# Kernel optimization log

Measured on AMD Instinct MI355X. Metric: run time of the kernel, lower is better.

The kernel has to match this reference:

```python
import jax, jax.numpy as jnp
import numpy as np

OBS_LEN = 8
B = 262144
H = 16   # lstm hidden / MADE hidden / cond dim
D = 2    # trajectory input dim / flow dim
N_FLOWS = 4
CLAMP = 5.0


def _masks():
    # MADE masks for num_inputs=2, num_hidden=16 (ikostrikov get_mask)
    in_deg = jnp.arange(D) % D                      # [0, 1]
    hid_deg = jnp.zeros((H,), jnp.float32)          # arange(16) % (2-1) == 0
    out_deg = (jnp.arange(2 * D) % D - 1).astype(jnp.float32)  # [-1,0,-1,0]
    input_mask = (hid_deg[:, None] >= in_deg[None, :].astype(jnp.float32)).astype(jnp.float32)  # [16,2]
    hidden_mask = jnp.ones((H, H), jnp.float32)     # all degrees 0 -> full
    output_mask = (out_deg[:, None] >= hid_deg[None, :]).astype(jnp.float32)  # [4,16]
    return input_mask, hidden_mask, output_mask


def _made_ma(x, cond, p, masks):
    # x: [B,2], cond: [B,16] -> m, a: [B,2]
    im, hm, om = masks
    jW, jb, cW, hW, hb, oW, ob = p
    h = x @ (jW * im).T + jb + cond @ cW.T      # joiner (masked) + cond linear (no bias)
    h = jax.nn.relu(h)
    h = jax.nn.relu(h @ (hW * hm).T + hb)       # trunk hidden masked linear
    out = h @ (oW * om).T + ob                  # trunk output masked linear -> [B,4]
    m, a = out[:, :D], out[:, D:]
    a = CLAMP * jnp.tanh(a / CLAMP)             # soft log-scale clamp (clamp_flow)
    return m, a


def _made_inverse(u, cond, p, masks):
    x = jnp.zeros_like(u)
    for i in range(D):
        m, a = _made_ma(x, cond, p, masks)
        x = x.at[:, i].set(u[:, i] * jnp.exp(a[:, i]) + m[:, i])
    return x


def _maf_sample(noise, cond, made_params, masks):
    # modules = [MADE0,Rev,MADE1,Rev,MADE2,Rev,MADE3,Rev]; sample runs inverse in reversed order
    x = noise
    for k in reversed(range(N_FLOWS)):
        x = x[:, ::-1]                           # Reverse(2) inverse == flip
        p = tuple(t[k] for t in made_params)
        x = _made_inverse(x, cond, p, masks)
    return x


def _encode(traj, enc_W, enc_b, W_ih, W_hh, b_ih, b_hh, h0, c0):
    # obs_len LSTM loop; dropout is identity in eval/test mode
    def step(carry, x_t):
        h, c = carry
        e = jax.nn.relu(x_t @ enc_W.T + enc_b)                 # [B,16]
        g = e @ W_ih.T + b_ih + h @ W_hh.T + b_hh              # [B,64]
        i, f, gg, o = jnp.split(g, 4, axis=-1)                 # torch LSTMCell gate order
        c = jax.nn.sigmoid(f) * c + jax.nn.sigmoid(i) * jnp.tanh(gg)
        h = jax.nn.sigmoid(o) * jnp.tanh(c)
        return (h, c), None
    (h, c), _ = jax.lax.scan(step, (h0, c0), traj)
    return h


def setup_inputs() -> dict:
    key = jax.random.key(0)
    ks = jax.random.split(key, 16)
    s = 0.1
    return {
        "traj_rel": jax.random.normal(ks[0], (OBS_LEN + 1, B, D), jnp.float32),
        "obs_traj_pos": jax.random.normal(ks[1], (OBS_LEN, B, D), jnp.float32),
        "h0": jax.random.normal(ks[2], (B, H), jnp.float32),
        "c0": jax.random.normal(ks[3], (B, H), jnp.float32),
        "noise": jax.random.normal(ks[4], (B, D), jnp.float32),
        "enc_W": jax.random.normal(ks[5], (H, D), jnp.float32) * 0.2,
        "enc_b": jnp.zeros((H,), jnp.float32),
        "lstm_W_ih": jax.random.normal(ks[6], (4 * H, H), jnp.float32) * s,
        "lstm_W_hh": jax.random.normal(ks[7], (4 * H, H), jnp.float32) * 0.001,
        "lstm_b_ih": jnp.zeros((4 * H,), jnp.float32).at[H:2 * H].set(1.0),
        "lstm_b_hh": jnp.zeros((4 * H,), jnp.float32),
        "made_joiner_W": jax.random.normal(ks[8], (N_FLOWS, H, D), jnp.float32) * s,
        "made_joiner_b": jnp.zeros((N_FLOWS, H), jnp.float32),
        "made_cond_W": jax.random.normal(ks[9], (N_FLOWS, H, H), jnp.float32) * s,
        "made_hid_W": jax.random.normal(ks[10], (N_FLOWS, H, H), jnp.float32) * s,
        "made_hid_b": jnp.zeros((N_FLOWS, H), jnp.float32),
        "made_out_W": jax.random.normal(ks[11], (N_FLOWS, 2 * D, H), jnp.float32) * s,
        "made_out_b": jnp.zeros((N_FLOWS, 2 * D), jnp.float32),
    }


def reference(traj_rel, obs_traj_pos, h0, c0, noise,
              enc_W, enc_b, lstm_W_ih, lstm_W_hh, lstm_b_ih, lstm_b_hh,
              made_joiner_W, made_joiner_b, made_cond_W,
              made_hid_W, made_hid_b, made_out_W, made_out_b):
    masks = _masks()
    h = _encode(traj_rel[:OBS_LEN], enc_W, enc_b,
                lstm_W_ih, lstm_W_hh, lstm_b_ih, lstm_b_hh, h0, c0)  # [B,16]
    made_params = (made_joiner_W, made_joiner_b, made_cond_W,
                   made_hid_W, made_hid_b, made_out_W, made_out_b)
    goal = _maf_sample(noise, h, made_params, masks)                  # [B,2]
    return goal + obs_traj_pos[-1]                                    # mode='test' output_pred
```

## Files before the change

### kernel.cpp

```cpp
#include <hip/hip_runtime.h>

#define B_N 262144
#define OBS_N 8

typedef __attribute__((ext_vector_type(4))) _Float16 f16x4;
typedef __attribute__((ext_vector_type(2))) __fp16 fp16x2;
typedef __attribute__((ext_vector_type(4))) float f32x4;

#define LOG2E 1.44269504088896340736f

__device__ __forceinline__ float rcpf_(float x){ return __builtin_amdgcn_rcpf(x); }
__device__ __forceinline__ float exp2f_(float x){ return __builtin_amdgcn_exp2f(x); }
__device__ __forceinline__ float expf_(float x){ return exp2f_(LOG2E * x); }
__device__ __forceinline__ float tanh_(float x){ return fmaf(-2.0f, rcpf_(exp2f_((2.0f*LOG2E) * x) + 1.0f), 1.0f); }

__device__ __forceinline__ f16x4 pack4(float a, float b, float c, float d){
    fp16x2 lo = __builtin_amdgcn_cvt_pkrtz(a, b);
    fp16x2 hi = __builtin_amdgcn_cvt_pkrtz(c, d);
    f16x4 r;
    r[0] = (_Float16)lo[0]; r[1] = (_Float16)lo[1];
    r[2] = (_Float16)hi[0]; r[3] = (_Float16)hi[1];
    return r;
}

#define MFMA16(a, b, c) __builtin_amdgcn_mfma_f32_16x16x16f16((a), (b), (c), 0, 0, 0)


__global__ __launch_bounds__(256) void goal_kernel(
    const float* __restrict__ traj,
    const float* __restrict__ obsp,
    const float* __restrict__ h0,
    const float* __restrict__ c0,
    const float* __restrict__ noise,
    const float* __restrict__ encW,
    const float* __restrict__ encb,
    const float* __restrict__ Wih,
    const float* __restrict__ Whh,
    const float* __restrict__ bih,
    const float* __restrict__ bhh,
    const float* __restrict__ jW,
    const float* __restrict__ jb,
    const float* __restrict__ cW,
    const float* __restrict__ hW,
    const float* __restrict__ hb,
    const float* __restrict__ oW,
    const float* __restrict__ ob,
    float* __restrict__ out)
{
    const int lane = threadIdx.x & 63;
    const int wv   = threadIdx.x >> 6;
    const int q    = lane >> 4;
    const int s    = lane & 15;
    const int j4   = q * 4;
    const int base = blockIdx.x * 128 + wv * 32;
    const int colA = base + s;
    const int colB = base + 16 + s;

    float ew0[4], ew1[4], eb[4];
    #pragma unroll
    for (int r = 0; r < 4; ++r) {
        ew0[r] = encW[(j4 + r) * 2 + 0];
        ew1[r] = encW[(j4 + r) * 2 + 1];
        eb[r]  = encb[j4 + r];
    }

    const float gsc[4] = { -LOG2E, -LOG2E, -2.0f*LOG2E, -LOG2E };

    f16x4 wihA[4], whhA[4];
    f32x4 bias[4];
    #pragma unroll
    for (int m = 0; m < 4; ++m) {
        float4 wa = *(const float4*)(Wih + (16 * m + s) * 16 + j4);
        float4 wb = *(const float4*)(Whh + (16 * m + s) * 16 + j4);
        wihA[m] = pack4(wa.x*gsc[m], wa.y*gsc[m], wa.z*gsc[m], wa.w*gsc[m]);
        whhA[m] = pack4(wb.x*gsc[m], wb.y*gsc[m], wb.z*gsc[m], wb.w*gsc[m]);
        float4 b1 = *(const float4*)(bih + 16 * m + j4);
        float4 b2 = *(const float4*)(bhh + 16 * m + j4);
        f32x4 bv;
        bv[0] = (b1.x + b2.x)*gsc[m]; bv[1] = (b1.y + b2.y)*gsc[m];
        bv[2] = (b1.z + b2.z)*gsc[m]; bv[3] = (b1.w + b2.w)*gsc[m];
        bias[m] = bv;
    }

    float ob0c[4], ob1c[4], ob2c[4], ob3c[4], ea0c[4];
    #pragma unroll
    for (int kf = 0; kf < 4; ++kf) {
        ob0c[kf] = ob[kf*4 + 0];
        ob1c[kf] = ob[kf*4 + 1];
        ob2c[kf] = ob[kf*4 + 2];
        ob3c[kf] = ob[kf*4 + 3] * 0.2f;
        ea0c[kf] = expf_(5.0f * tanh_(ob2c[kf] * 0.2f));
    }

    f32x4 cA = *(const f32x4*)(c0 + colA * 16 + j4);
    f32x4 cB = *(const f32x4*)(c0 + colB * 16 + j4);
    float4 hA0 = *(const float4*)(h0 + colA * 16 + j4);
    float4 hB0 = *(const float4*)(h0 + colB * 16 + j4);
    f16x4 hA = pack4(hA0.x, hA0.y, hA0.z, hA0.w);
    f16x4 hB = pack4(hB0.x, hB0.y, hB0.z, hB0.w);

    float2 nzA = *(const float2*)(noise + colA * 2);
    float2 nzB = *(const float2*)(noise + colB * 2);

    float2 xA = *(const float2*)(traj + colA * 2);
    float2 xB = *(const float2*)(traj + colB * 2);

    const float NEG2L2E = -2.0f * LOG2E;

    for (int t = 0; t < OBS_N; ++t) {
        float2 nxA, nxB;
        if (t < OBS_N - 1) {
            nxA = *(const float2*)(traj + (t + 1) * (B_N * 2) + colA * 2);
            nxB = *(const float2*)(traj + (t + 1) * (B_N * 2) + colB * 2);
        }
        float eAv[4], eBv[4];
        #pragma unroll
        for (int r = 0; r < 4; ++r) {
            eAv[r] = fmaxf(fmaf(ew0[r], xA.x, fmaf(ew1[r], xA.y, eb[r])), 0.0f);
            eBv[r] = fmaxf(fmaf(ew0[r], xB.x, fmaf(ew1[r], xB.y, eb[r])), 0.0f);
        }
        f16x4 eA = pack4(eAv[0], eAv[1], eAv[2], eAv[3]);
        f16x4 eB = pack4(eBv[0], eBv[1], eBv[2], eBv[3]);

        f32x4 gA[4], gB[4];
        #pragma unroll
        for (int m = 0; m < 4; ++m) {
            gA[m] = MFMA16(wihA[m], eA, bias[m]);
            gA[m] = MFMA16(whhA[m], hA, gA[m]);
            gB[m] = MFMA16(wihA[m], eB, bias[m]);
            gB[m] = MFMA16(whhA[m], hB, gB[m]);
        }

        float hnA[4], hnB[4];
        #pragma unroll
        for (int r = 0; r < 4; ++r) {
            {
                float Ei = exp2f_(gA[0][r]);
                float Ef = exp2f_(gA[1][r]);
                float Eg = exp2f_(gA[2][r]);
                float Eo = exp2f_(gA[3][r]);
                float pi = 1.0f + Ei, pf = 1.0f + Ef, pg = 1.0f + Eg;
                float m_ = pi * pg;
                float R1 = rcpf_(m_ * pf);
                float cn = fmaf(cA[r], m_, (1.0f - Eg) * pf) * R1;
                cA[r] = cn;
                float Ec = exp2f_(NEG2L2E * cn);
                float R2 = rcpf_((1.0f + Ec) * (1.0f + Eo));
                hnA[r] = (1.0f - Ec) * R2;
            }
            {
                float Ei = exp2f_(gB[0][r]);
                float Ef = exp2f_(gB[1][r]);
                float Eg = exp2f_(gB[2][r]);
                float Eo = exp2f_(gB[3][r]);
                float pi = 1.0f + Ei, pf = 1.0f + Ef, pg = 1.0f + Eg;
                float m_ = pi * pg;
                float R1 = rcpf_(m_ * pf);
                float cn = fmaf(cB[r], m_, (1.0f - Eg) * pf) * R1;
                cB[r] = cn;
                float Ec = exp2f_(NEG2L2E * cn);
                float R2 = rcpf_((1.0f + Ec) * (1.0f + Eo));
                hnB[r] = (1.0f - Ec) * R2;
            }
        }
        hA = pack4(hnA[0], hnA[1], hnA[2], hnA[3]);
        hB = pack4(hnB[0], hnB[1], hnB[2], hnB[3]);

        if (t < OBS_N - 1) { xA = nxA; xB = nxB; }
    }

    float2 ppA = *(const float2*)(obsp + (OBS_N - 1) * (B_N * 2) + colA * 2);
    float2 ppB = *(const float2*)(obsp + (OBS_N - 1) * (B_N * 2) + colB * 2);

    float x0A = nzA.x, x1A = nzA.y;
    float x0B = nzB.x, x1B = nzB.y;

    #pragma unroll
    for (int kf = 3; kf >= 0; --kf) {
        float tA = x0A; x0A = x1A; x1A = tA;
        float tB = x0B; x0B = x1B; x1B = tB;

        float4 cw = *(const float4*)(cW + kf * 256 + s * 16 + j4);
        f16x4 cwA = pack4(cw.x, cw.y, cw.z, cw.w);
        float4 hw = *(const float4*)(hW + kf * 256 + s * 16 + j4);
        f16x4 hwA = pack4(hw.x, hw.y, hw.z, hw.w);
        {
        }
        float osc = ((s & 3) == 3) ? 0.2f : 1.0f;
        float4 ow = *(const float4*)(oW + kf * 64 + (s & 3) * 16 + j4);
        f16x4 owA = pack4(ow.x * osc, ow.y * osc, ow.z * osc, ow.w * osc);

        float jw0[4], jb_[4], hb_[4];
        #pragma unroll
        for (int r = 0; r < 4; ++r) {
            jw0[r] = jW[kf * 32 + (j4 + r) * 2];
            jb_[r] = jb[kf * 16 + j4 + r];
            hb_[r] = hb[kf * 16 + j4 + r];
        }

        x0A = fmaf(x0A, ea0c[kf], ob0c[kf]);
        x0B = fmaf(x0B, ea0c[kf], ob0c[kf]);

        f32x4 a1A, a1B;
        #pragma unroll
        for (int r = 0; r < 4; ++r) {
            a1A[r] = fmaf(jw0[r], x0A, jb_[r]);
            a1B[r] = fmaf(jw0[r], x0B, jb_[r]);
        }
        a1A = MFMA16(cwA, hA, a1A);
        a1B = MFMA16(cwA, hB, a1B);
        f16x4 h1A = pack4(fmaxf(a1A[0],0.f), fmaxf(a1A[1],0.f), fmaxf(a1A[2],0.f), fmaxf(a1A[3],0.f));
        f16x4 h1B = pack4(fmaxf(a1B[0],0.f), fmaxf(a1B[1],0.f), fmaxf(a1B[2],0.f), fmaxf(a1B[3],0.f));

        f32x4 a2A, a2B;
        #pragma unroll
        for (int r = 0; r < 4; ++r) { a2A[r] = hb_[r]; a2B[r] = hb_[r]; }
        a2A = MFMA16(hwA, h1A, a2A);
        a2B = MFMA16(hwA, h1B, a2B);
        f16x4 h2A = pack4(fmaxf(a2A[0],0.f), fmaxf(a2A[1],0.f), fmaxf(a2A[2],0.f), fmaxf(a2A[3],0.f));
        f16x4 h2B = pack4(fmaxf(a2B[0],0.f), fmaxf(a2B[1],0.f), fmaxf(a2B[2],0.f), fmaxf(a2B[3],0.f));

        f32x4 a3A, a3B;
        a3A[0]=ob0c[kf]; a3A[1]=ob1c[kf]; a3A[2]=ob2c[kf]; a3A[3]=ob3c[kf];
        a3B[0]=ob0c[kf]; a3B[1]=ob1c[kf]; a3B[2]=ob2c[kf]; a3B[3]=ob3c[kf];
        a3A = MFMA16(owA, h2A, a3A);
        a3B = MFMA16(owA, h2B, a3B);

        float a1vA = 5.0f * tanh_(a3A[3]);
        float a1vB = 5.0f * tanh_(a3B[3]);
        x1A = fmaf(x1A, expf_(a1vA), a3A[1]);
        x1B = fmaf(x1B, expf_(a1vB), a3B[1]);
    }

    if (q == 0) {
        float2 oA; oA.x = x0A + ppA.x; oA.y = x1A + ppA.y;
        float2 oB; oB.x = x0B + ppB.x; oB.y = x1B + ppB.y;
        *(float2*)(out + colA * 2) = oA;
        *(float2*)(out + colB * 2) = oB;
    }
}

extern "C" void kernel_launch(void* const* d_in, const int* in_sizes, int n_in,
                              void* d_out, int out_size, void* d_ws, size_t ws_size,
                              hipStream_t stream) {
    goal_kernel<<<B_N / 128, 256, 0, stream>>>(
        (const float*)d_in[0],  (const float*)d_in[1],  (const float*)d_in[2],
        (const float*)d_in[3],  (const float*)d_in[4],  (const float*)d_in[5],
        (const float*)d_in[6],  (const float*)d_in[7],  (const float*)d_in[8],
        (const float*)d_in[9],  (const float*)d_in[10], (const float*)d_in[11],
        (const float*)d_in[12], (const float*)d_in[13], (const float*)d_in[14],
        (const float*)d_in[15], (const float*)d_in[16], (const float*)d_in[17],
        (float*)d_out);
}
```

Baseline: 50.22 us.

## Cut register pressure: fp16 encoder math, rolled loops, occupancy launch bound

Adds a launch bound of four blocks per CU and marks the LSTM and flow loops as not unrolled. Encoder weights and gate biases are stored as packed fp16, and the encoder affine plus ReLU runs in packed half math. Per-flow output-bias constants are recomputed inside the flow loop, and the final position load moves into the q==0 branch. The aim is fewer VGPRs and higher occupancy, at the cost of lower encoder precision and lost cross-iteration scheduling freedom from unrolling.

New measurement: 44.32 us, median of 3. 11.8% less time.

```diff
diff --git a/kernel.cpp b/kernel.cpp
--- a/kernel.cpp
+++ b/kernel.cpp
@@ -11,7 +11,6 @@
 
 __device__ __forceinline__ float rcpf_(float x){ return __builtin_amdgcn_rcpf(x); }
 __device__ __forceinline__ float exp2f_(float x){ return __builtin_amdgcn_exp2f(x); }
-__device__ __forceinline__ float expf_(float x){ return exp2f_(LOG2E * x); }
 __device__ __forceinline__ float tanh_(float x){ return fmaf(-2.0f, rcpf_(exp2f_((2.0f*LOG2E) * x) + 1.0f), 1.0f); }
 
 __device__ __forceinline__ f16x4 pack4(float a, float b, float c, float d){
@@ -25,8 +24,7 @@
 
 #define MFMA16(a, b, c) __builtin_amdgcn_mfma_f32_16x16x16f16((a), (b), (c), 0, 0, 0)
 
-
-__global__ __launch_bounds__(256) void goal_kernel(
+__global__ __launch_bounds__(256, 4) void goal_kernel(
     const float* __restrict__ traj,
     const float* __restrict__ obsp,
     const float* __restrict__ h0,
@@ -56,18 +54,17 @@
     const int colA = base + s;
     const int colB = base + 16 + s;
 
-    float ew0[4], ew1[4], eb[4];
+    f16x4 ew0h, ew1h, ebh;
     #pragma unroll
     for (int r = 0; r < 4; ++r) {
-        ew0[r] = encW[(j4 + r) * 2 + 0];
-        ew1[r] = encW[(j4 + r) * 2 + 1];
-        eb[r]  = encb[j4 + r];
+        ew0h[r] = (_Float16)encW[(j4 + r) * 2 + 0];
+        ew1h[r] = (_Float16)encW[(j4 + r) * 2 + 1];
+        ebh[r]  = (_Float16)encb[j4 + r];
     }
 
     const float gsc[4] = { -LOG2E, -LOG2E, -2.0f*LOG2E, -LOG2E };
 
-    f16x4 wihA[4], whhA[4];
-    f32x4 bias[4];
+    f16x4 wihA[4], whhA[4], biasH[4];
     #pragma unroll
     for (int m = 0; m < 4; ++m) {
         float4 wa = *(const float4*)(Wih + (16 * m + s) * 16 + j4);
@@ -76,20 +73,8 @@
         whhA[m] = pack4(wb.x*gsc[m], wb.y*gsc[m], wb.z*gsc[m], wb.w*gsc[m]);
         float4 b1 = *(const float4*)(bih + 16 * m + j4);
         float4 b2 = *(const float4*)(bhh + 16 * m + j4);
-        f32x4 bv;
-        bv[0] = (b1.x + b2.x)*gsc[m]; bv[1] = (b1.y + b2.y)*gsc[m];
-        bv[2] = (b1.z + b2.z)*gsc[m]; bv[3] = (b1.w + b2.w)*gsc[m];
-        bias[m] = bv;
-    }
-
-    float ob0c[4], ob1c[4], ob2c[4], ob3c[4], ea0c[4];
-    #pragma unroll
-    for (int kf = 0; kf < 4; ++kf) {
-        ob0c[kf] = ob[kf*4 + 0];
-        ob1c[kf] = ob[kf*4 + 1];
-        ob2c[kf] = ob[kf*4 + 2];
-        ob3c[kf] = ob[kf*4 + 3] * 0.2f;
-        ea0c[kf] = expf_(5.0f * tanh_(ob2c[kf] * 0.2f));
+        biasH[m] = pack4((b1.x+b2.x)*gsc[m], (b1.y+b2.y)*gsc[m],
+                         (b1.z+b2.z)*gsc[m], (b1.w+b2.w)*gsc[m]);
     }
 
     f32x4 cA = *(const f32x4*)(c0 + colA * 16 + j4);
@@ -102,32 +87,40 @@
     float2 nzA = *(const float2*)(noise + colA * 2);
     float2 nzB = *(const float2*)(noise + colB * 2);
 
+    const float NEG2L2E = -2.0f * LOG2E;
+
     float2 xA = *(const float2*)(traj + colA * 2);
     float2 xB = *(const float2*)(traj + colB * 2);
 
-    const float NEG2L2E = -2.0f * LOG2E;
-
+    #pragma unroll 1
     for (int t = 0; t < OBS_N; ++t) {
         float2 nxA, nxB;
         if (t < OBS_N - 1) {
             nxA = *(const float2*)(traj + (t + 1) * (B_N * 2) + colA * 2);
             nxB = *(const float2*)(traj + (t + 1) * (B_N * 2) + colB * 2);
         }
-        float eAv[4], eBv[4];
+
+        _Float16 ax = (_Float16)xA.x, ay = (_Float16)xA.y;
+        _Float16 bx = (_Float16)xB.x, by = (_Float16)xB.y;
+        f16x4 xxA = { ax, ax, ax, ax }, yyA = { ay, ay, ay, ay };
+        f16x4 xxB = { bx, bx, bx, bx }, yyB = { by, by, by, by };
+        f16x4 eA = ew0h * xxA + ew1h * yyA + ebh;
+        f16x4 eB = ew0h * xxB + ew1h * yyB + ebh;
         #pragma unroll
         for (int r = 0; r < 4; ++r) {
-            eAv[r] = fmaxf(fmaf(ew0[r], xA.x, fmaf(ew1[r], xA.y, eb[r])), 0.0f);
-            eBv[r] = fmaxf(fmaf(ew0[r], xB.x, fmaf(ew1[r], xB.y, eb[r])), 0.0f);
-        }
-        f16x4 eA = pack4(eAv[0], eAv[1], eAv[2], eAv[3]);
-        f16x4 eB = pack4(eBv[0], eBv[1], eBv[2], eBv[3]);
+            eA[r] = eA[r] > (_Float16)0 ? eA[r] : (_Float16)0;
+            eB[r] = eB[r] > (_Float16)0 ? eB[r] : (_Float16)0;
+        }
 
         f32x4 gA[4], gB[4];
         #pragma unroll
         for (int m = 0; m < 4; ++m) {
-            gA[m] = MFMA16(wihA[m], eA, bias[m]);
+            f32x4 bv;
+            bv[0] = (float)biasH[m][0]; bv[1] = (float)biasH[m][1];
+            bv[2] = (float)biasH[m][2]; bv[3] = (float)biasH[m][3];
+            gA[m] = MFMA16(wihA[m], eA, bv);
             gA[m] = MFMA16(whhA[m], hA, gA[m]);
-            gB[m] = MFMA16(wihA[m], eB, bias[m]);
+            gB[m] = MFMA16(wihA[m], eB, bv);
             gB[m] = MFMA16(whhA[m], hB, gB[m]);
         }
 
@@ -139,28 +132,28 @@
                 float Ef = exp2f_(gA[1][r]);
                 float Eg = exp2f_(gA[2][r]);
                 float Eo = exp2f_(gA[3][r]);
-                float pi = 1.0f + Ei, pf = 1.0f + Ef, pg = 1.0f + Eg;
+                float pi = 1.0f + Ei, pg = 1.0f + Eg, pf = 1.0f + Ef;
                 float m_ = pi * pg;
                 float R1 = rcpf_(m_ * pf);
-                float cn = fmaf(cA[r], m_, (1.0f - Eg) * pf) * R1;
+                float cn = fmaf(cA[r], m_, fmaf(-Eg, pf, pf)) * R1;
                 cA[r] = cn;
                 float Ec = exp2f_(NEG2L2E * cn);
                 float R2 = rcpf_((1.0f + Ec) * (1.0f + Eo));
-                hnA[r] = (1.0f - Ec) * R2;
+                hnA[r] = fmaf(-Ec, R2, R2);
             }
             {
                 float Ei = exp2f_(gB[0][r]);
                 float Ef = exp2f_(gB[1][r]);
                 float Eg = exp2f_(gB[2][r]);
                 float Eo = exp2f_(gB[3][r]);
-                float pi = 1.0f + Ei, pf = 1.0f + Ef, pg = 1.0f + Eg;
+                float pi = 1.0f + Ei, pg = 1.0f + Eg, pf = 1.0f + Ef;
                 float m_ = pi * pg;
                 float R1 = rcpf_(m_ * pf);
-                float cn = fmaf(cB[r], m_, (1.0f - Eg) * pf) * R1;
+                float cn = fmaf(cB[r], m_, fmaf(-Eg, pf, pf)) * R1;
                 cB[r] = cn;
                 float Ec = exp2f_(NEG2L2E * cn);
                 float R2 = rcpf_((1.0f + Ec) * (1.0f + Eo));
-                hnB[r] = (1.0f - Ec) * R2;
+                hnB[r] = fmaf(-Ec, R2, R2);
             }
         }
         hA = pack4(hnA[0], hnA[1], hnA[2], hnA[3]);
@@ -169,43 +162,35 @@
         if (t < OBS_N - 1) { xA = nxA; xB = nxB; }
     }
 
-    float2 ppA = *(const float2*)(obsp + (OBS_N - 1) * (B_N * 2) + colA * 2);
-    float2 ppB = *(const float2*)(obsp + (OBS_N - 1) * (B_N * 2) + colB * 2);
-
     float x0A = nzA.x, x1A = nzA.y;
     float x0B = nzB.x, x1B = nzB.y;
 
-    #pragma unroll
+    #pragma unroll 1
     for (int kf = 3; kf >= 0; --kf) {
         float tA = x0A; x0A = x1A; x1A = tA;
         float tB = x0B; x0B = x1B; x1B = tB;
+
+        float ob0 = ob[kf*4 + 0], ob1 = ob[kf*4 + 1];
+        float ob2 = ob[kf*4 + 2], ob3 = ob[kf*4 + 3] * 0.2f;
+        float ea0 = exp2f_(7.2134752044f * tanh_(ob2 * 0.2f));
+        x0A = fmaf(x0A, ea0, ob0);
+        x0B = fmaf(x0B, ea0, ob0);
 
         float4 cw = *(const float4*)(cW + kf * 256 + s * 16 + j4);
         f16x4 cwA = pack4(cw.x, cw.y, cw.z, cw.w);
         float4 hw = *(const float4*)(hW + kf * 256 + s * 16 + j4);
         f16x4 hwA = pack4(hw.x, hw.y, hw.z, hw.w);
-        {
-        }
         float osc = ((s & 3) == 3) ? 0.2f : 1.0f;
         float4 ow = *(const float4*)(oW + kf * 64 + (s & 3) * 16 + j4);
         f16x4 owA = pack4(ow.x * osc, ow.y * osc, ow.z * osc, ow.w * osc);
 
-        float jw0[4], jb_[4], hb_[4];
+        f32x4 a1A, a1B;
         #pragma unroll
         for (int r = 0; r < 4; ++r) {
-            jw0[r] = jW[kf * 32 + (j4 + r) * 2];
-            jb_[r] = jb[kf * 16 + j4 + r];
-            hb_[r] = hb[kf * 16 + j4 + r];
-        }
-
-        x0A = fmaf(x0A, ea0c[kf], ob0c[kf]);
-        x0B = fmaf(x0B, ea0c[kf], ob0c[kf]);
-
-        f32x4 a1A, a1B;
-        #pragma unroll
-        for (int r = 0; r < 4; ++r) {
-            a1A[r] = fmaf(jw0[r], x0A, jb_[r]);
-            a1B[r] = fmaf(jw0[r], x0B, jb_[r]);
+            float jwv = jW[kf * 32 + (j4 + r) * 2];
+            float jbv = jb[kf * 16 + j4 + r];
+            a1A[r] = fmaf(jwv, x0A, jbv);
+            a1B[r] = fmaf(jwv, x0B, jbv);
         }
         a1A = MFMA16(cwA, hA, a1A);
         a1B = MFMA16(cwA, hB, a1B);
@@ -214,25 +199,25 @@
 
         f32x4 a2A, a2B;
         #pragma unroll
-        for (int r = 0; r < 4; ++r) { a2A[r] = hb_[r]; a2B[r] = hb_[r]; }
+        for (int r = 0; r < 4; ++r) { float hbv = hb[kf * 16 + j4 + r]; a2A[r] = hbv; a2B[r] = hbv; }
         a2A = MFMA16(hwA, h1A, a2A);
         a2B = MFMA16(hwA, h1B, a2B);
         f16x4 h2A = pack4(fmaxf(a2A[0],0.f), fmaxf(a2A[1],0.f), fmaxf(a2A[2],0.f), fmaxf(a2A[3],0.f));
         f16x4 h2B = pack4(fmaxf(a2B[0],0.f), fmaxf(a2B[1],0.f), fmaxf(a2B[2],0.f), fmaxf(a2B[3],0.f));
 
         f32x4 a3A, a3B;
-        a3A[0]=ob0c[kf]; a3A[1]=ob1c[kf]; a3A[2]=ob2c[kf]; a3A[3]=ob3c[kf];
-        a3B[0]=ob0c[kf]; a3B[1]=ob1c[kf]; a3B[2]=ob2c[kf]; a3B[3]=ob3c[kf];
+        a3A[0] = ob0; a3A[1] = ob1; a3A[2] = ob2; a3A[3] = ob3;
+        a3B = a3A;
         a3A = MFMA16(owA, h2A, a3A);
         a3B = MFMA16(owA, h2B, a3B);
 
-        float a1vA = 5.0f * tanh_(a3A[3]);
-        float a1vB = 5.0f * tanh_(a3B[3]);
-        x1A = fmaf(x1A, expf_(a1vA), a3A[1]);
-        x1B = fmaf(x1B, expf_(a1vB), a3B[1]);
+        x1A = fmaf(x1A, exp2f_(7.2134752044f * tanh_(a3A[3])), a3A[1]);
+        x1B = fmaf(x1B, exp2f_(7.2134752044f * tanh_(a3B[3])), a3B[1]);
     }
 
     if (q == 0) {
+        float2 ppA = *(const float2*)(obsp + (OBS_N - 1) * (B_N * 2) + colA * 2);
+        float2 ppB = *(const float2*)(obsp + (OBS_N - 1) * (B_N * 2) + colB * 2);
         float2 oA; oA.x = x0A + ppA.x; oA.y = x1A + ppA.y;
         float2 oB; oB.x = x0B + ppB.x; oB.y = x1B + ppB.y;
         *(float2*)(out + colA * 2) = oA;
```
